# Kernel optimization log

Hardware: AMD Instinct MI355X
Metric: run time of the kernel (lower is better)

The kernel has to match this reference:

```python
import jax, jax.numpy as jnp
import numpy as np

S, B, D, H = 256, 32, 512, 512

def setup_inputs() -> dict:
    key = jax.random.key(0)
    ks = jax.random.split(key, 14)
    return {
        "x": jax.random.normal(ks[0], (S, B, D), jnp.float32),
        "hidden_prev": jax.random.normal(ks[1], (1, B, H), jnp.float32) * 0.1,
        "Z_state": jax.random.normal(ks[2], (1, B, H, D), jnp.float32) * 0.01,
        "F_state": jax.random.normal(ks[3], (1, B, H, D), jnp.float32) * 0.01,
        "wz_state": jax.random.normal(ks[4], (1, B, H), jnp.float32) * 0.01,
        "wf_state": jax.random.normal(ks[5], (1, B, H), jnp.float32) * 0.01,
        "bz_state": jax.random.normal(ks[6], (1, B, H), jnp.float32) * 0.01,
        "bf_state": jax.random.normal(ks[7], (1, B, H), jnp.float32) * 0.01,
        "wm_z": jax.random.normal(ks[8], (H, D), jnp.float32) * 0.1,
        "wm_f": jax.random.normal(ks[9], (H, D), jnp.float32) * 0.1,
        "wv_z": jax.random.normal(ks[10], (1, H), jnp.float32) * 0.1,
        "wv_f": jax.random.normal(ks[11], (1, H), jnp.float32) * 0.1,
        "bias_z": jax.random.normal(ks[12], (1, H), jnp.float32) * 0.1,
        "bias_f": jax.random.normal(ks[13], (1, H), jnp.float32) * 0.1,
    }

def reference(x, hidden_prev, Z_state, F_state, wz_state, wf_state, bz_state, bf_state,
              wm_z, wm_f, wv_z, wv_f, bias_z, bias_f):
    # Input projections for both gates, done once: [S,B,H]
    pre_z = jnp.einsum('sbd,hd->sbh', x, wm_z)
    pre_f = jnp.einsum('sbd,hd->sbh', x, wm_f)

    def step(carry, inp):
        cell, Z, Fm, wz, wf, bz, bf = carry
        x_t, pz, pf = inp  # [B,D], [B,H], [B,H]
        z = jnp.tanh(pz + wv_z * cell + bias_z)          # [B,H]
        f = jax.nn.sigmoid(pf + wv_f * cell + bias_f)    # [B,H]
        zf = (1.0 - f) * (1.0 - z * z)
        fz = (cell - z) * (1.0 - f) * f
        common = f + zf * wv_z + fz * wv_f
        # RTRL sensitivity updates (outer products over [B,H,D])
        Zn = common[..., None] * Z + zf[..., None] * x_t[:, None, :]
        Fn = common[..., None] * Fm + fz[..., None] * x_t[:, None, :]
        wzn = cell * zf + common * wz
        wfn = cell * fz + common * wf
        bzn = zf + common * bz
        bfn = fz + common * bf
        new_cell = cell * f + (1.0 - f) * z
        return (new_cell, Zn, Fn, wzn, wfn, bzn, bfn), new_cell

    carry0 = (hidden_prev[0], Z_state[0], F_state[0],
              wz_state[0], wf_state[0], bz_state[0], bf_state[0])
    carry, cells = jax.lax.scan(step, carry0, (x, pre_z, pre_f))
    new_cell, Zn, Fn, wzn, wfn, bzn, bfn = carry
    return (cells, new_cell[None], Zn[None], Fn[None],
            wzn[None], wfn[None], bzn[None], bfn[None])
```

## Files before the change

kernel.cpp:

```cpp
#include <hip/hip_runtime.h>
#include <math.h>

namespace {

typedef short short8 __attribute__((ext_vector_type(8)));
typedef float floatx4 __attribute__((ext_vector_type(4)));
typedef unsigned int uint32;
typedef unsigned short u16;
typedef unsigned long long u64;

constexpr int S = 256, B = 32, D = 512, H = 512;
constexpr int BH = B * H;
constexpr int M1 = S * B;
constexpr int WN = H * D;
constexpr int SBH = S * BH;

__device__ __forceinline__ int swz(int row, int col8) {
  return row * 64 + (col8 ^ ((row & 7) << 3));
}

__device__ __forceinline__ uint32 f2bf(float f) {
  uint32 x = __float_as_uint(f);
  return (x + 0x7fffu + ((x >> 16) & 1u)) >> 16;
}

__device__ __forceinline__ float fast_sigmoid(float x) {
  float e = __expf(-x);
  return __builtin_amdgcn_rcpf(1.0f + e);
}
__device__ __forceinline__ float fast_tanh(float x) {
  float e = __expf(-2.0f * x);
  return fmaf(2.0f, __builtin_amdgcn_rcpf(1.0f + e), -1.0f);
}

__global__ __launch_bounds__(256) void convert_w(
    const float* __restrict__ wmz, const float* __restrict__ wmf,
    u16* __restrict__ wmzb, u16* __restrict__ wmfb) {
  int i = (blockIdx.x * 256 + threadIdx.x) * 8;
  const float* src;
  u16* dst;
  int off;
  if (i < WN) {
    src = wmz; dst = wmzb; off = i;
  } else {
    src = wmf; dst = wmfb; off = i - WN;
  }
  float4 a = *(const float4*)&src[off];
  float4 b = *(const float4*)&src[off + 4];
  uint4 o;
  o.x = f2bf(a.x) | (f2bf(a.y) << 16);
  o.y = f2bf(a.z) | (f2bf(a.w) << 16);
  o.z = f2bf(b.x) | (f2bf(b.y) << 16);
  o.w = f2bf(b.z) | (f2bf(b.w) << 16);
  *(uint4*)&dst[off] = o;
}

__global__ __launch_bounds__(256) void xpose_kernel(
    const float* __restrict__ x, u16* __restrict__ XT) {
  __shared__ float lds[64][65];
  const int s0 = blockIdx.x * 64;
  const int d0 = blockIdx.y * 64;
  const int b = blockIdx.z;
  const int r = threadIdx.x >> 4;
  const int c4 = (threadIdx.x & 15) * 4;
#pragma unroll
  for (int p = 0; p < 4; ++p) {
    const int rr = r + p * 16;
    float4 v = *(const float4*)&x[(size_t)(s0 + rr) * (B * D) +
                                  (size_t)b * D + d0 + c4];
    lds[c4 + 0][rr] = v.x;
    lds[c4 + 1][rr] = v.y;
    lds[c4 + 2][rr] = v.z;
    lds[c4 + 3][rr] = v.w;
  }
  __syncthreads();
#pragma unroll
  for (int p = 0; p < 4; ++p) {
    const int dr = r + p * 16;
    const float v0 = lds[dr][c4 + 0];
    const float v1 = lds[dr][c4 + 1];
    const float v2 = lds[dr][c4 + 2];
    const float v3 = lds[dr][c4 + 3];
    u64 o = (u64)f2bf(v0) | ((u64)f2bf(v1) << 16) | ((u64)f2bf(v2) << 32) |
            ((u64)f2bf(v3) << 48);
    *(u64*)&XT[((size_t)b * D + d0 + dr) * S + s0 + c4] = o;
  }
}

__global__ __launch_bounds__(256) void proj_gemm(
    const float* __restrict__ x, const u16* __restrict__ wmzb,
    const u16* __restrict__ wmfb, float2* __restrict__ pzf) {
  __shared__ u16 As[128 * 64];
  __shared__ u16 Bzs[64 * 64];
  __shared__ u16 Bfs[64 * 64];
  const int tid = threadIdx.x;
  const int m0 = blockIdx.x * 128;
  const int n0 = blockIdx.y * 64;
  const int w = tid >> 6, l = tid & 63;
  const int lr = l & 15, lg = l >> 4;
  floatx4 accz[2][4], accf[2][4];
#pragma unroll
  for (int m = 0; m < 2; ++m)
#pragma unroll
    for (int n = 0; n < 4; ++n) {
      accz[m][n] = 0;
      accf[m][n] = 0;
    }
  const int sr = tid >> 3;
  const int sc = (tid & 7) * 8;
  for (int k0 = 0; k0 < D; k0 += 64) {
    __syncthreads();
#pragma unroll
    for (int p = 0; p < 4; ++p) {
      const int r = sr + 32 * p;
      const float* xp = &x[(size_t)(m0 + r) * D + k0 + sc];
      float4 a = *(const float4*)xp;
      float4 b = *(const float4*)(xp + 4);
      uint4 o;
      o.x = f2bf(a.x) | (f2bf(a.y) << 16);
      o.y = f2bf(a.z) | (f2bf(a.w) << 16);
      o.z = f2bf(b.x) | (f2bf(b.y) << 16);
      o.w = f2bf(b.z) | (f2bf(b.w) << 16);
      *(uint4*)&As[swz(r, sc)] = o;
    }
#pragma unroll
    for (int p = 0; p < 2; ++p) {
      const int r = sr + 32 * p;
      *(short8*)&Bzs[swz(r, sc)] =
          *(const short8*)&wmzb[(size_t)(n0 + r) * D + k0 + sc];
      *(short8*)&Bfs[swz(r, sc)] =
          *(const short8*)&wmfb[(size_t)(n0 + r) * D + k0 + sc];
    }
    __syncthreads();
#pragma unroll
    for (int kk = 0; kk < 2; ++kk) {
      const int kb = kk * 32 + lg * 8;
      short8 a0 = *(const short8*)&As[swz(32 * w + lr, kb)];
      short8 a1 = *(const short8*)&As[swz(32 * w + 16 + lr, kb)];
#pragma unroll
      for (int n = 0; n < 4; ++n) {
        short8 bz = *(const short8*)&Bzs[swz(16 * n + lr, kb)];
        short8 bf = *(const short8*)&Bfs[swz(16 * n + lr, kb)];
        accz[0][n] = __builtin_amdgcn_mfma_f32_16x16x32_bf16(a0, bz, accz[0][n], 0, 0, 0);
        accz[1][n] = __builtin_amdgcn_mfma_f32_16x16x32_bf16(a1, bz, accz[1][n], 0, 0, 0);
        accf[0][n] = __builtin_amdgcn_mfma_f32_16x16x32_bf16(a0, bf, accf[0][n], 0, 0, 0);
        accf[1][n] = __builtin_amdgcn_mfma_f32_16x16x32_bf16(a1, bf, accf[1][n], 0, 0, 0);
      }
    }
  }
#pragma unroll
  for (int m = 0; m < 2; ++m)
#pragma unroll
    for (int n = 0; n < 4; ++n)
#pragma unroll
      for (int j = 0; j < 4; ++j) {
        int row = m0 + 32 * w + 16 * m + lg * 4 + j;
        int col = n0 + 16 * n + lr;
        pzf[(size_t)row * H + col] = make_float2(accz[m][n][j], accf[m][n][j]);
      }
}

#define STEP_BODY(J)                                                       \
    const float z = fast_tanh(fmaf(wvz, cell, pzv));                       \
    const float f = fast_sigmoid(fmaf(wvf, cell, pfv));                    \
    const float zf = (1.0f - f) * (1.0f - z * z);                          \
    const float fz = (cell - z) * (1.0f - f) * f;                          \
    const float common = f + zf * wvz + fz * wvf;                          \
    wz = fmaf(common, wz, cell * zf);                                      \
    wf = fmaf(common, wf, cell * fz);                                      \
    bz = fmaf(common, bz, zf);                                             \
    bf = fmaf(common, bf, fz);                                             \
    cell = fmaf(f, cell - z, z);                                           \
    const size_t ti = (size_t)(t0 + (J)) * BH;                             \
    cp[ti] = cell;                                                         \
    pz[ti] = make_float2(                                                  \
        __uint_as_float(f2bf(zf) | (f2bf(fz) << 16)), common);

#define STEP_L(J, Q)                                                       \
  {                                                                        \
    const float pzv = Q.x + bsz, pfv = Q.y + bsf;                          \
    Q = pz[(size_t)(t0 + 16 + (J)) * BH];                                  \
    STEP_BODY(J)                                                           \
  }

#define STEP_N(J, Q)                                                       \
  {                                                                        \
    const float pzv = Q.x + bsz, pfv = Q.y + bsf;                          \
    STEP_BODY(J)                                                           \
  }

__global__ __launch_bounds__(64, 1) void scan_fwd(
    const float* __restrict__ hidden_prev, const float* __restrict__ wz0,
    const float* __restrict__ wf0, const float* __restrict__ bz0,
    const float* __restrict__ bf0, const float* __restrict__ wvz_,
    const float* __restrict__ wvf_, const float* __restrict__ bsz_,
    const float* __restrict__ bsf_, float2* pzf_,
    float* __restrict__ out_cells, float* __restrict__ out_newcell,
    float* __restrict__ out_wzn, float* __restrict__ out_wfn,
    float* __restrict__ out_bzn, float* __restrict__ out_bfn) {
  const int bh = blockIdx.x * 64 + threadIdx.x;
  const int h = bh & (H - 1);
  float cell = hidden_prev[bh];
  float wz = wz0[bh], wf = wf0[bh], bz = bz0[bh], bf = bf0[bh];
  const float wvz = wvz_[h], wvf = wvf_[h], bsz = bsz_[h], bsf = bsf_[h];
  float2* pz = pzf_ + bh;
  float* cp = out_cells + bh;

  float2 q0 = pz[(size_t)0 * BH], q1 = pz[(size_t)1 * BH];
  float2 q2 = pz[(size_t)2 * BH], q3 = pz[(size_t)3 * BH];
  float2 q4 = pz[(size_t)4 * BH], q5 = pz[(size_t)5 * BH];
  float2 q6 = pz[(size_t)6 * BH], q7 = pz[(size_t)7 * BH];
  float2 q8 = pz[(size_t)8 * BH], q9 = pz[(size_t)9 * BH];
  float2 q10 = pz[(size_t)10 * BH], q11 = pz[(size_t)11 * BH];
  float2 q12 = pz[(size_t)12 * BH], q13 = pz[(size_t)13 * BH];
  float2 q14 = pz[(size_t)14 * BH], q15 = pz[(size_t)15 * BH];

  for (int t0 = 0; t0 < S - 16; t0 += 16) {
    STEP_L(0, q0)  STEP_L(1, q1)  STEP_L(2, q2)  STEP_L(3, q3)
    STEP_L(4, q4)  STEP_L(5, q5)  STEP_L(6, q6)  STEP_L(7, q7)
    STEP_L(8, q8)  STEP_L(9, q9)  STEP_L(10, q10) STEP_L(11, q11)
    STEP_L(12, q12) STEP_L(13, q13) STEP_L(14, q14) STEP_L(15, q15)
  }
  {
    const int t0 = S - 16;
    STEP_N(0, q0)  STEP_N(1, q1)  STEP_N(2, q2)  STEP_N(3, q3)
    STEP_N(4, q4)  STEP_N(5, q5)  STEP_N(6, q6)  STEP_N(7, q7)
    STEP_N(8, q8)  STEP_N(9, q9)  STEP_N(10, q10) STEP_N(11, q11)
    STEP_N(12, q12) STEP_N(13, q13) STEP_N(14, q14) STEP_N(15, q15)
  }
  out_newcell[bh] = cell;
  out_wzn[bh] = wz;
  out_wfn[bh] = wf;
  out_bzn[bh] = bz;
  out_bfn[bh] = bf;
}

__global__ __launch_bounds__(1024) void suffix_kernel(
    const float2* __restrict__ pzfc, u16* __restrict__ AzT,
    u16* __restrict__ AfT, float* __restrict__ P0_out) {
  __shared__ float prods[16][65];
  __shared__ uint32 tl[S * 65];
  const int bh_l = threadIdx.x & 63;
  const int c = threadIdx.x >> 6;
  const int bh = blockIdx.x * 64 + bh_l;
  const float2* p = pzfc + bh;
  float2 v[16];
#pragma unroll
  for (int i = 0; i < 16; ++i) v[i] = p[(size_t)(c * 16 + i) * BH];
  float L = 1.0f;
#pragma unroll
  for (int i = 0; i < 16; ++i) L *= v[i].y;
  prods[c][bh_l] = L;
  __syncthreads();
  float run = 1.0f;
#pragma unroll
  for (int cc = 1; cc < 16; ++cc)
    if (cc > c) run *= prods[cc][bh_l];
#pragma unroll
  for (int i = 15; i >= 0; --i) {
    const int t = c * 16 + i;
    const uint32 w32 = __float_as_uint(v[i].x);
    const float zf = __uint_as_float((w32 & 0xffffu) << 16);
    const float fz = __uint_as_float(w32 & 0xffff0000u);
    tl[t * 65 + bh_l] = f2bf(zf * run) | (f2bf(fz * run) << 16);
    run *= v[i].y;
  }
  if (c == 0) P0_out[bh] = run;
  __syncthreads();
  const size_t base = (size_t)blockIdx.x * 64 * S;
#pragma unroll
  for (int it = 0; it < 4; ++it) {
    const int qi = it * 1024 + threadIdx.x;
    const int r = qi >> 6;
    const int qt = (qi & 63) * 4;
    const uint32 a0 = tl[(qt + 0) * 65 + r];
    const uint32 a1 = tl[(qt + 1) * 65 + r];
    const uint32 a2 = tl[(qt + 2) * 65 + r];
    const uint32 a3 = tl[(qt + 3) * 65 + r];
    u64 lo = (u64)(a0 & 0xffffu) | ((u64)(a1 & 0xffffu) << 16) |
             ((u64)(a2 & 0xffffu) << 32) | ((u64)(a3 & 0xffffu) << 48);
    u64 hi = (u64)(a0 >> 16) | ((u64)(a1 >> 16) << 16) |
             ((u64)(a2 >> 16) << 32) | ((u64)(a3 >> 16) << 48);
    *(u64*)&AzT[base + (size_t)r * S + qt] = lo;
    *(u64*)&AfT[base + (size_t)r * S + qt] = hi;
  }
}

__global__ __launch_bounds__(256, 3) void out_gemm(
    const u16* __restrict__ AzT, const u16* __restrict__ AfT,
    const u16* __restrict__ XT, const float* __restrict__ P0,
    const float* __restrict__ Z0, const float* __restrict__ F0,
    float* __restrict__ Zn, float* __restrict__ Fn) {
  __shared__ u16 smem[2][(128 + 64) * 64];
  const int tid = threadIdx.x;
  const int h0 = blockIdx.x * 128;
  const int d0 = blockIdx.y * 64;
  const int bz = blockIdx.z;
  const int b = bz >> 1;
  const u16* A = ((bz & 1) ? AfT : AzT) + (size_t)b * H * S;
  const float* C0 = (bz & 1) ? F0 : Z0;
  float* Cn = (bz & 1) ? Fn : Zn;
  const u16* Xb = XT + (size_t)b * D * S;
  const int w = tid >> 6, l = tid & 63;
  const int lr = l & 15, lg = l >> 4;
  floatx4 acc[2][4];
#pragma unroll
  for (int m = 0; m < 2; ++m)
#pragma unroll
    for (int n = 0; n < 4; ++n) acc[m][n] = 0;
  const int sr = tid >> 3;
  const int sc = (tid & 7) * 8;

  short8 rA[4], rX[2];

#define OG_LOAD(T0)                                                        \
  {                                                                        \
    _Pragma("unroll") for (int p = 0; p < 4; ++p) {                        \
      const int r = sr + 32 * p;                                           \
      rA[p] = *(const short8*)&A[(size_t)(h0 + r) * S + (T0) + sc];        \
    }                                                                      \
    _Pragma("unroll") for (int p = 0; p < 2; ++p) {                        \
      const int r = sr + 32 * p;                                           \
      rX[p] = *(const short8*)&Xb[(size_t)(d0 + r) * S + (T0) + sc];       \
    }                                                                      \
  }

#define OG_WRITE(BUF)                                                      \
  {                                                                        \
    u16* As_ = smem[BUF];                                                  \
    u16* Xs_ = smem[BUF] + 128 * 64;                                       \
    _Pragma("unroll") for (int p = 0; p < 4; ++p) {                        \
      const int r = sr + 32 * p;                                           \
      *(short8*)&As_[swz(r, sc)] = rA[p];                                  \
    }                                                                      \
    _Pragma("unroll") for (int p = 0; p < 2; ++p) {                        \
      const int r = sr + 32 * p;                                           \
      *(short8*)&Xs_[swz(r, sc)] = rX[p];                                  \
    }                                                                      \
  }

#define OG_COMPUTE(BUF)                                                    \
  {                                                                        \
    const u16* As_ = smem[BUF];                                            \
    const u16* Xs_ = smem[BUF] + 128 * 64;                                 \
    _Pragma("unroll") for (int kk = 0; kk < 2; ++kk) {                     \
      const int kb = kk * 32 + lg * 8;                                     \
      short8 a0 = *(const short8*)&As_[swz(32 * w + lr, kb)];              \
      short8 a1 = *(const short8*)&As_[swz(32 * w + 16 + lr, kb)];         \
      _Pragma("unroll") for (int n = 0; n < 4; ++n) {                      \
        short8 xf = *(const short8*)&Xs_[swz(16 * n + lr, kb)];            \
        acc[0][n] = __builtin_amdgcn_mfma_f32_16x16x32_bf16(a0, xf, acc[0][n], 0, 0, 0); \
        acc[1][n] = __builtin_amdgcn_mfma_f32_16x16x32_bf16(a1, xf, acc[1][n], 0, 0, 0); \
      }                                                                    \
    }                                                                      \
  }

  OG_LOAD(0)
  OG_WRITE(0)
  __syncthreads();
  OG_LOAD(64)
  OG_COMPUTE(0)
  OG_WRITE(1)
  __syncthreads();
  OG_LOAD(128)
  OG_COMPUTE(1)
  OG_WRITE(0)
  __syncthreads();
  OG_LOAD(192)
  OG_COMPUTE(0)
  OG_WRITE(1)
  __syncthreads();
  OG_COMPUTE(1)

  __syncthreads();
  float* eps = (float*)&smem[0][0];
#pragma unroll
  for (int m = 0; m < 2; ++m)
#pragma unroll
    for (int n = 0; n < 4; ++n)
#pragma unroll
      for (int j = 0; j < 4; ++j) {
        const int row = 32 * w + 16 * m + lg * 4 + j;
        eps[row * 68 + 16 * n + lr] = acc[m][n][j];
      }
  __syncthreads();
#pragma unroll
  for (int i = 0; i < 8; ++i) {
    const int id = i * 256 + tid;
    const int row = id >> 4;
    const int c4 = (id & 15) * 4;
    const int h = h0 + row;
    const float p0 = P0[b * H + h];
    const size_t gi = ((size_t)b * H + h) * D + d0 + c4;
    const float4 a = *(const float4*)&eps[row * 68 + c4];
    const float4 c0 = *(const float4*)&C0[gi];
    float4 o;
    o.x = fmaf(p0, c0.x, a.x);
    o.y = fmaf(p0, c0.y, a.y);
    o.z = fmaf(p0, c0.z, a.z);
    o.w = fmaf(p0, c0.w, a.w);
    *(float4*)&Cn[gi] = o;
  }
#undef OG_LOAD
#undef OG_WRITE
#undef OG_COMPUTE
}

}

extern "C" void kernel_launch(void* const* d_in, const int* in_sizes, int n_in,
                              void* d_out, int out_size, void* d_ws,
                              size_t ws_size, hipStream_t stream) {
  const float* x = (const float*)d_in[0];
  const float* hidden_prev = (const float*)d_in[1];
  const float* Z_state = (const float*)d_in[2];
  const float* F_state = (const float*)d_in[3];
  const float* wz_state = (const float*)d_in[4];
  const float* wf_state = (const float*)d_in[5];
  const float* bz_state = (const float*)d_in[6];
  const float* bf_state = (const float*)d_in[7];
  const float* wm_z = (const float*)d_in[8];
  const float* wm_f = (const float*)d_in[9];
  const float* wv_z = (const float*)d_in[10];
  const float* wv_f = (const float*)d_in[11];
  const float* bias_z = (const float*)d_in[12];
  const float* bias_f = (const float*)d_in[13];

  float2* pzf = (float2*)d_ws;
  u16* AzT = (u16*)(pzf + SBH);
  u16* AfT = AzT + SBH;
  u16* XT = AfT + SBH;
  u16* wmzb = XT + SBH;
  u16* wmfb = wmzb + WN;
  float* P0 = (float*)(wmfb + WN);

  float* out = (float*)d_out;
  float* out_cells = out;
  float* out_newcell = out + SBH;
  float* out_Zn = out_newcell + BH;
  float* out_Fn = out_Zn + (size_t)BH * D;
  float* out_wzn = out_Fn + (size_t)BH * D;
  float* out_wfn = out_wzn + BH;
  float* out_bzn = out_wfn + BH;
  float* out_bfn = out_bzn + BH;

  convert_w<<<2 * WN / 8 / 256, 256, 0, stream>>>(wm_z, wm_f, wmzb, wmfb);
  xpose_kernel<<<dim3(S / 64, D / 64, B), 256, 0, stream>>>(x, XT);
  proj_gemm<<<dim3(M1 / 128, H / 64), 256, 0, stream>>>(x, wmzb, wmfb, pzf);
  scan_fwd<<<BH / 64, 64, 0, stream>>>(
      hidden_prev, wz_state, wf_state, bz_state, bf_state, wv_z, wv_f, bias_z,
      bias_f, pzf, out_cells, out_newcell, out_wzn, out_wfn, out_bzn,
      out_bfn);
  suffix_kernel<<<BH / 64, 1024, 0, stream>>>(pzf, AzT, AfT, P0);
  out_gemm<<<dim3(H / 128, D / 64, B * 2), 256, 0, stream>>>(
      AzT, AfT, XT, P0, Z_state, F_state, out_Zn, out_Fn);
}
```

Before: 105.5 us.

## Merge prep kernels, add MFMA priority hints, prefetch epilogue state loads

Merges the weight bf16 conversion and the x transpose into one launch by dispatching on block index, which removes one kernel launch. Wraps the MFMA loops in proj_gemm and out_gemm with s_setprio so compute waves get issue priority. In out_gemm, the C0 and P0 epilogue loads are issued before the final compute stage so their latency overlaps the MFMAs. This raises register pressure in out_gemm.

```diff
diff --git a/kernel.cpp b/kernel.cpp
--- a/kernel.cpp
+++ b/kernel.cpp
@@ -33,57 +33,59 @@
   return fmaf(2.0f, __builtin_amdgcn_rcpf(1.0f + e), -1.0f);
 }
 
-__global__ __launch_bounds__(256) void convert_w(
-    const float* __restrict__ wmz, const float* __restrict__ wmf,
+__global__ __launch_bounds__(256) void prep_kernel(
+    const float* __restrict__ x, const float* __restrict__ wmz,
+    const float* __restrict__ wmf, u16* __restrict__ XT,
     u16* __restrict__ wmzb, u16* __restrict__ wmfb) {
-  int i = (blockIdx.x * 256 + threadIdx.x) * 8;
-  const float* src;
-  u16* dst;
-  int off;
-  if (i < WN) {
-    src = wmz; dst = wmzb; off = i;
+  __shared__ float lds[64][65];
+  const int bid = blockIdx.x;
+  if (bid < 1024) {
+    const int b = bid >> 5;
+    const int rem = bid & 31;
+    const int d0 = (rem >> 2) * 64;
+    const int s0 = (rem & 3) * 64;
+    const int r = threadIdx.x >> 4;
+    const int c4 = (threadIdx.x & 15) * 4;
+#pragma unroll
+    for (int p = 0; p < 4; ++p) {
+      const int rr = r + p * 16;
+      float4 v = *(const float4*)&x[(size_t)(s0 + rr) * (B * D) +
+                                    (size_t)b * D + d0 + c4];
+      lds[c4 + 0][rr] = v.x;
+      lds[c4 + 1][rr] = v.y;
+      lds[c4 + 2][rr] = v.z;
+      lds[c4 + 3][rr] = v.w;
+    }
+    __syncthreads();
+#pragma unroll
+    for (int p = 0; p < 4; ++p) {
+      const int dr = r + p * 16;
+      const float v0 = lds[dr][c4 + 0];
+      const float v1 = lds[dr][c4 + 1];
+      const float v2 = lds[dr][c4 + 2];
+      const float v3 = lds[dr][c4 + 3];
+      u64 o = (u64)f2bf(v0) | ((u64)f2bf(v1) << 16) | ((u64)f2bf(v2) << 32) |
+              ((u64)f2bf(v3) << 48);
+      *(u64*)&XT[((size_t)b * D + d0 + dr) * S + s0 + c4] = o;
+    }
   } else {
-    src = wmf; dst = wmfb; off = i - WN;
-  }
-  float4 a = *(const float4*)&src[off];
-  float4 b = *(const float4*)&src[off + 4];
-  uint4 o;
-  o.x = f2bf(a.x) | (f2bf(a.y) << 16);
-  o.y = f2bf(a.z) | (f2bf(a.w) << 16);
-  o.z = f2bf(b.x) | (f2bf(b.y) << 16);
-  o.w = f2bf(b.z) | (f2bf(b.w) << 16);
-  *(uint4*)&dst[off] = o;
-}
-
-__global__ __launch_bounds__(256) void xpose_kernel(
-    const float* __restrict__ x, u16* __restrict__ XT) {
-  __shared__ float lds[64][65];
-  const int s0 = blockIdx.x * 64;
-  const int d0 = blockIdx.y * 64;
-  const int b = blockIdx.z;
-  const int r = threadIdx.x >> 4;
-  const int c4 = (threadIdx.x & 15) * 4;
-#pragma unroll
-  for (int p = 0; p < 4; ++p) {
-    const int rr = r + p * 16;
-    float4 v = *(const float4*)&x[(size_t)(s0 + rr) * (B * D) +
-                                  (size_t)b * D + d0 + c4];
-    lds[c4 + 0][rr] = v.x;
-    lds[c4 + 1][rr] = v.y;
-    lds[c4 + 2][rr] = v.z;
-    lds[c4 + 3][rr] = v.w;
-  }
-  __syncthreads();
-#pragma unroll
-  for (int p = 0; p < 4; ++p) {
-    const int dr = r + p * 16;
-    const float v0 = lds[dr][c4 + 0];
-    const float v1 = lds[dr][c4 + 1];
-    const float v2 = lds[dr][c4 + 2];
-    const float v3 = lds[dr][c4 + 3];
-    u64 o = (u64)f2bf(v0) | ((u64)f2bf(v1) << 16) | ((u64)f2bf(v2) << 32) |
-            ((u64)f2bf(v3) << 48);
-    *(u64*)&XT[((size_t)b * D + d0 + dr) * S + s0 + c4] = o;
+    int i = ((bid - 1024) * 256 + threadIdx.x) * 8;
+    const float* src;
+    u16* dst;
+    int off;
+    if (i < WN) {
+      src = wmz; dst = wmzb; off = i;
+    } else {
+      src = wmf; dst = wmfb; off = i - WN;
+    }
+    float4 a = *(const float4*)&src[off];
+    float4 b4 = *(const float4*)&src[off + 4];
+    uint4 o;
+    o.x = f2bf(a.x) | (f2bf(a.y) << 16);
+    o.y = f2bf(a.z) | (f2bf(a.w) << 16);
+    o.z = f2bf(b4.x) | (f2bf(b4.y) << 16);
+    o.w = f2bf(b4.z) | (f2bf(b4.w) << 16);
+    *(uint4*)&dst[off] = o;
   }
 }
 
@@ -132,6 +134,7 @@
           *(const short8*)&wmfb[(size_t)(n0 + r) * D + k0 + sc];
     }
     __syncthreads();
+    __builtin_amdgcn_s_setprio(1);
 #pragma unroll
     for (int kk = 0; kk < 2; ++kk) {
       const int kb = kk * 32 + lg * 8;
@@ -147,6 +150,7 @@
         accf[1][n] = __builtin_amdgcn_mfma_f32_16x16x32_bf16(a1, bf, accf[1][n], 0, 0, 0);
       }
     }
+    __builtin_amdgcn_s_setprio(0);
   }
 #pragma unroll
   for (int m = 0; m < 2; ++m)
@@ -343,6 +347,7 @@
   {                                                                        \
     const u16* As_ = smem[BUF];                                            \
     const u16* Xs_ = smem[BUF] + 128 * 64;                                 \
+    __builtin_amdgcn_s_setprio(1);                                         \
     _Pragma("unroll") for (int kk = 0; kk < 2; ++kk) {                     \
       const int kb = kk * 32 + lg * 8;                                     \
       short8 a0 = *(const short8*)&As_[swz(32 * w + lr, kb)];              \
@@ -353,6 +358,7 @@
         acc[1][n] = __builtin_amdgcn_mfma_f32_16x16x32_bf16(a1, xf, acc[1][n], 0, 0, 0); \
       }                                                                    \
     }                                                                      \
+    __builtin_amdgcn_s_setprio(0);                                         \
   }
 
   OG_LOAD(0)
@@ -370,35 +376,46 @@
   OG_COMPUTE(0)
   OG_WRITE(1)
   __syncthreads();
-  OG_COMPUTE(1)
-
-  __syncthreads();
-  float* eps = (float*)&smem[0][0];
-#pragma unroll
-  for (int m = 0; m < 2; ++m)
-#pragma unroll
-    for (int n = 0; n < 4; ++n)
-#pragma unroll
-      for (int j = 0; j < 4; ++j) {
-        const int row = 32 * w + 16 * m + lg * 4 + j;
-        eps[row * 68 + 16 * n + lr] = acc[m][n][j];
-      }
-  __syncthreads();
+
+  float4 c0v[8];
+  float p0v[8];
 #pragma unroll
   for (int i = 0; i < 8; ++i) {
     const int id = i * 256 + tid;
     const int row = id >> 4;
     const int c4 = (id & 15) * 4;
     const int h = h0 + row;
-    const float p0 = P0[b * H + h];
+    p0v[i] = P0[b * H + h];
+    c0v[i] = *(const float4*)&C0[((size_t)b * H + h) * D + d0 + c4];
+  }
+
+  OG_COMPUTE(1)
+
+  __syncthreads();
+  float* eps = (float*)&smem[0][0];
+#pragma unroll
+  for (int m = 0; m < 2; ++m)
+#pragma unroll
+    for (int n = 0; n < 4; ++n)
+#pragma unroll
+      for (int j = 0; j < 4; ++j) {
+        const int row = 32 * w + 16 * m + lg * 4 + j;
+        eps[row * 68 + 16 * n + lr] = acc[m][n][j];
+      }
+  __syncthreads();
+#pragma unroll
+  for (int i = 0; i < 8; ++i) {
+    const int id = i * 256 + tid;
+    const int row = id >> 4;
+    const int c4 = (id & 15) * 4;
+    const int h = h0 + row;
     const size_t gi = ((size_t)b * H + h) * D + d0 + c4;
     const float4 a = *(const float4*)&eps[row * 68 + c4];
-    const float4 c0 = *(const float4*)&C0[gi];
     float4 o;
-    o.x = fmaf(p0, c0.x, a.x);
-    o.y = fmaf(p0, c0.y, a.y);
-    o.z = fmaf(p0, c0.z, a.z);
-    o.w = fmaf(p0, c0.w, a.w);
+    o.x = fmaf(p0v[i], c0v[i].x, a.x);
+    o.y = fmaf(p0v[i], c0v[i].y, a.y);
+    o.z = fmaf(p0v[i], c0v[i].z, a.z);
+    o.w = fmaf(p0v[i], c0v[i].w, a.w);
     *(float4*)&Cn[gi] = o;
   }
 #undef OG_LOAD
@@ -444,8 +461,7 @@
   float* out_bzn = out_wfn + BH;
   float* out_bfn = out_bzn + BH;
 
-  convert_w<<<2 * WN / 8 / 256, 256, 0, stream>>>(wm_z, wm_f, wmzb, wmfb);
-  xpose_kernel<<<dim3(S / 64, D / 64, B), 256, 0, stream>>>(x, XT);
+  prep_kernel<<<1024 + 256, 256, 0, stream>>>(x, wm_z, wm_f, XT, wmzb, wmfb);
   proj_gemm<<<dim3(M1 / 128, H / 64), 256, 0, stream>>>(x, wmzb, wmfb, pzf);
   scan_fwd<<<BH / 64, 64, 0, stream>>>(
       hidden_prev, wz_state, wf_state, bz_state, bf_state, wv_z, wv_f, bias_z,
```

New measurement: 101.9 us. 1.04x faster.
